# Kernel tuning notes

Measured on AMD Instinct MI355X. Metric: run time of the kernel, lower is better.

Reference implementation:

```python
import jax, jax.numpy as jnp
import numpy as np

ALPHA = 0.2          # LeakyReLU negative slope
THRESHOLD = 0.5      # adjacency threshold
NEG_INF = -9e15      # same fill value as torch source


def setup_inputs() -> dict:
    key = jax.random.key(0)
    k_in, k_adj, k_W, k_a = jax.random.split(key, 4)
    B, N, C = 32, 1024, 64
    inp = jax.random.normal(k_in, (B, N, C), dtype=jnp.float32)
    adj = jax.random.uniform(k_adj, (N, N), dtype=jnp.float32)
    # xavier_uniform with gain=1.414 (as in torch init)
    gain = 1.414
    lim_W = gain * np.sqrt(6.0 / (C + C))
    W = jax.random.uniform(k_W, (C, C), dtype=jnp.float32, minval=-lim_W, maxval=lim_W)
    lim_a = gain * np.sqrt(6.0 / (2 * C + 1))
    a = jax.random.uniform(k_a, (2 * C, 1), dtype=jnp.float32, minval=-lim_a, maxval=lim_a)
    return {"input": inp, "adj": adj, "W": W, "a": a}


def reference(input, adj, W, a):
    # h: [B, N, C]
    h = jnp.matmul(input, W)
    C = W.shape[0]
    a_src = a[:C, 0]   # applied to h_i (row / query node)
    a_dst = a[C:, 0]   # applied to h_j (col / neighbor node)
    # Algebraic decomposition of a^T [h_i || h_j]: outer-sum of two [B,N] vectors.
    s_src = jnp.matmul(h, a_src)  # [B, N]
    s_dst = jnp.matmul(h, a_dst)  # [B, N]
    e = jax.nn.leaky_relu(s_src[:, :, None] + s_dst[:, None, :], negative_slope=ALPHA)  # [B,N,N]
    mask = adj > THRESHOLD  # [N, N], broadcast over batch
    attention = jax.nn.softmax(jnp.where(mask[None, :, :], e, NEG_INF), axis=2)
    h_prime = jnp.matmul(attention, h)  # [B, N, C]
    return jax.nn.elu(h_prime)
```

## Files before the change

kernel.cpp:

```cpp
#include <hip/hip_runtime.h>
#include <math.h>

#define ALPHA 0.2f

constexpr int B = 32, N = 1024, C = 64;
constexpr int TI = 16;
constexpr int TJ = 64;

typedef __attribute__((ext_vector_type(8))) short short8;
typedef __attribute__((ext_vector_type(4))) float floatx4;

static __device__ __forceinline__ unsigned f32bf(float f) {
    unsigned u = __float_as_uint(f);
    return (u + 0x7FFFu + ((u >> 16) & 1u)) >> 16;
}

__global__ __launch_bounds__(256) void gat_mask(const float* __restrict__ adj,
                                                const float* __restrict__ Wm,
                                                const float* __restrict__ a,
                                                unsigned long long* __restrict__ mask64,
                                                float* __restrict__ wa)
{
    const int lane = threadIdx.x & 63;
    const int wave = threadIdx.x >> 6;
    const int id   = blockIdx.x * 4 + wave;
    const int i    = id >> 4;
    const int jc   = id & 15;
    const float av = adj[(size_t)i * N + jc * 64 + lane];
    const unsigned long long bal = __ballot(av > 0.5f);
    if (lane == 0) mask64[i * 16 + jc] = bal;

    if (blockIdx.x == 0 && wave == 0) {
        float accs = 0.f, accd = 0.f;
#pragma unroll
        for (int c4 = 0; c4 < 16; ++c4) {
            const float4 wv = *(const float4*)&Wm[lane * 64 + c4 * 4];
            const float4 as = *(const float4*)&a[c4 * 4];
            const float4 ad = *(const float4*)&a[64 + c4 * 4];
            accs = fmaf(wv.x, as.x, fmaf(wv.y, as.y, fmaf(wv.z, as.z, fmaf(wv.w, as.w, accs))));
            accd = fmaf(wv.x, ad.x, fmaf(wv.y, ad.y, fmaf(wv.z, ad.z, fmaf(wv.w, ad.w, accd))));
        }
        wa[lane] = accs;
        wa[64 + lane] = accd;
    }
}

__global__ __launch_bounds__(256) void gat_hs(const float* __restrict__ input,
                                              const float* __restrict__ Wm,
                                              const float* __restrict__ wa,
                                              unsigned short* __restrict__ hT,
                                              float* __restrict__ ssrc,
                                              float* __restrict__ sdst)
{
    __shared__ __align__(16) float ins[64 * 68];
    __shared__ __align__(16) unsigned short hsT[64 * 72];
    __shared__ float red_s[256], red_d[256];
    __shared__ float wa_l[128];

    const int tid  = threadIdx.x;
    const int lane = tid & 63;
    const int wave = tid >> 6;
    const int row0 = blockIdx.x * 64;
    const int b    = row0 >> 10;
    const int jb   = row0 & 1023;

    float wreg[64];
#pragma unroll
    for (int k = 0; k < 64; ++k) wreg[k] = Wm[k * 64 + lane];

    const float4* gin = (const float4*)(input + (size_t)row0 * 64);
#pragma unroll
    for (int s = 0; s < 4; ++s) {
        const int id = tid + 256 * s;
        *(float4*)&ins[(id >> 4) * 68 + (id & 15) * 4] = gin[id];
    }
    if (tid < 128) wa_l[tid] = wa[tid];
    __syncthreads();

    for (int r = 0; r < 16; ++r) {
        const int row = wave * 16 + r;
        float acc = 0.f;
#pragma unroll
        for (int k4 = 0; k4 < 16; ++k4) {
            const float4 iv = *(const float4*)&ins[row * 68 + k4 * 4];
            acc = fmaf(iv.x, wreg[k4 * 4 + 0], acc);
            acc = fmaf(iv.y, wreg[k4 * 4 + 1], acc);
            acc = fmaf(iv.z, wreg[k4 * 4 + 2], acc);
            acc = fmaf(iv.w, wreg[k4 * 4 + 3], acc);
        }
        hsT[lane * 72 + row] = (unsigned short)f32bf(acc);
    }

    {
        const int r = tid & 63, kq = tid >> 6;
        float as = 0.f, ad = 0.f;
#pragma unroll
        for (int t = 0; t < 4; ++t) {
            const float4 iv = *(const float4*)&ins[r * 68 + kq * 16 + t * 4];
            const float4 ws = *(const float4*)&wa_l[kq * 16 + t * 4];
            const float4 wd = *(const float4*)&wa_l[64 + kq * 16 + t * 4];
            as = fmaf(iv.x, ws.x, fmaf(iv.y, ws.y, fmaf(iv.z, ws.z, fmaf(iv.w, ws.w, as))));
            ad = fmaf(iv.x, wd.x, fmaf(iv.y, wd.y, fmaf(iv.z, wd.z, fmaf(iv.w, wd.w, ad))));
        }
        red_s[tid] = as;
        red_d[tid] = ad;
    }
    __syncthreads();

    if (tid < 64) {
        ssrc[row0 + tid] = red_s[tid] + red_s[tid + 64] + red_s[tid + 128] + red_s[tid + 192];
        sdst[row0 + tid] = red_d[tid] + red_d[tid + 64] + red_d[tid + 128] + red_d[tid + 192];
    }

    {
        const int c = tid >> 2, part = tid & 3;
        const short8 v0 = *(const short8*)&hsT[c * 72 + part * 16];
        const short8 v1 = *(const short8*)&hsT[c * 72 + part * 16 + 8];
        const size_t g = ((size_t)(b * 64 + c)) * 1024 + jb + part * 16;
        *(short8*)&hT[g] = v0;
        *(short8*)&hT[g + 8] = v1;
    }
}

__global__ __launch_bounds__(256) void gat_attn(const unsigned short* __restrict__ hTg,
                                                const float* __restrict__ ssrc,
                                                const float* __restrict__ sdst,
                                                const unsigned* __restrict__ mask32,
                                                float* __restrict__ out)
{
    __shared__ __align__(16) unsigned short h_u[64 * 64];
    __shared__ __align__(16) unsigned short p_u[16 * 64];
    __shared__ float psum_s[16];

    const int tid  = threadIdx.x;
    const int lane = tid & 63;
    const int wave = tid >> 6;
    const int b    = blockIdx.x & 31;
    const int i0   = (blockIdx.x >> 5) * TI;

    const int ii = tid >> 4;
    const int jq = tid & 15;
    const float ssq = ssrc[b * N + i0 + ii];
    const unsigned short* hTb = hTg + (size_t)b * 64 * 1024;
    const float* sd = sdst + b * N;
    const unsigned* mrow = mask32 + (size_t)(i0 + ii) * 32;

    const int c = tid >> 2, m2 = tid & 3;
    const int hw0 = c * 64 + (((m2 * 2)    ) ^ (c & 7)) * 8;
    const int hw1 = c * 64 + (((m2 * 2 + 1)) ^ (c & 7)) * 8;
    const int pwi = ii * 64 + ((jq >> 1) ^ (ii & 7)) * 8 + (jq & 1) * 4;
    const int fa_ii = lane & 15, fq = lane >> 4;
    const int cB = wave * 16 + (lane & 15);

    floatx4 acc = {0.f, 0.f, 0.f, 0.f};
    float psacc = 0.f;

    for (int jt = 0; jt < 16; ++jt) {
        const short8 g0 = *(const short8*)&hTb[(size_t)c * 1024 + jt * 64 + m2 * 16];
        const short8 g1 = *(const short8*)&hTb[(size_t)c * 1024 + jt * 64 + m2 * 16 + 8];
        const float4 sd4 = *(const float4*)&sd[jt * 64 + jq * 4];
        const unsigned bits = mrow[jt * 2 + (jq >> 3)] >> ((jq & 7) * 4);

        __syncthreads();
        *(short8*)&h_u[hw0] = g0;
        *(short8*)&h_u[hw1] = g1;

        float e0 = ssq + sd4.x; e0 = e0 > 0.f ? e0 : ALPHA * e0;
        float e1 = ssq + sd4.y; e1 = e1 > 0.f ? e1 : ALPHA * e1;
        float e2 = ssq + sd4.z; e2 = e2 > 0.f ? e2 : ALPHA * e2;
        float e3 = ssq + sd4.w; e3 = e3 > 0.f ? e3 : ALPHA * e3;
        const float p0 = (bits & 1u) ? __expf(e0) : 0.f;
        const float p1 = (bits & 2u) ? __expf(e1) : 0.f;
        const float p2 = (bits & 4u) ? __expf(e2) : 0.f;
        const float p3 = (bits & 8u) ? __expf(e3) : 0.f;
        psacc += (p0 + p1) + (p2 + p3);
        const uint2 pw = {f32bf(p0) | (f32bf(p1) << 16), f32bf(p2) | (f32bf(p3) << 16)};
        *(uint2*)&p_u[pwi] = pw;
        __syncthreads();

#pragma unroll
        for (int t = 0; t < 2; ++t) {
            const short8 af = *(const short8*)&p_u[fa_ii * 64 + ((t * 4 + fq) ^ (fa_ii & 7)) * 8];
            const short8 bf = *(const short8*)&h_u[cB * 64 + ((t * 4 + fq) ^ (cB & 7)) * 8];
            acc = __builtin_amdgcn_mfma_f32_16x16x32_bf16(af, bf, acc, 0, 0, 0);
        }
    }

#pragma unroll
    for (int off = 1; off < 16; off <<= 1) psacc += __shfl_xor(psacc, off, 64);
    if ((tid & 15) == 0) psum_s[ii] = psacc;
    __syncthreads();

#pragma unroll
    for (int r = 0; r < 4; ++r) {
        const int row = fq * 4 + r;
        const float hp = acc[r] / psum_s[row];
        const float o = hp > 0.f ? hp : __expf(hp) - 1.f;
        out[((size_t)(b * N + i0 + row)) * 64 + wave * 16 + (lane & 15)] = o;
    }
}

extern "C" void kernel_launch(void* const* d_in, const int* in_sizes, int n_in,
                              void* d_out, int out_size, void* d_ws, size_t ws_size,
                              hipStream_t stream) {
    const float* input = (const float*)d_in[0];
    const float* adj   = (const float*)d_in[1];
    const float* Wm    = (const float*)d_in[2];
    const float* a     = (const float*)d_in[3];
    float* out = (float*)d_out;

    char* ws = (char*)d_ws;
    unsigned short* hT = (unsigned short*)ws;
    float* ssrc = (float*)(ws + 4194304);
    float* sdst = (float*)(ws + 4194304 + 131072);
    unsigned long long* mask64 = (unsigned long long*)(ws + 4194304 + 2 * 131072);
    float* wa = (float*)(ws + 4194304 + 3 * 131072);

    gat_mask<<<N * N / 64 / 4, 256, 0, stream>>>(adj, Wm, a, mask64, wa);
    gat_hs<<<B * N / 64, 256, 0, stream>>>(input, Wm, wa, hT, ssrc, sdst);
    gat_attn<<<(N / TI) * B, 256, 0, stream>>>(hT, ssrc, sdst, (const unsigned*)mask64, out);
}
```

Before: 96.98 us.

## Split attention j-range across waves with register-direct MFMA operands and LDS reduction

The attention kernel is restructured so that each of the four waves handles a disjoint quarter of the neighbor tiles for all 64 output channels. Probabilities are built directly in MFMA A-operand registers and H tiles are loaded straight from global memory into B-operand registers, which removes the per-tile LDS staging and the two barriers per iteration. Partial accumulators and row sums are combined through shared memory once at the end. Scores are prescaled by log2(e) in the projection kernel so the hardware exp2 can be used, bf16 packing uses v_cvt_pk_bf16_f32, and the block-to-(batch,row) mapping is changed. The trade-offs are higher register pressure and uncoalesced strided global loads of H.

```diff
diff --git a/kernel.cpp b/kernel.cpp
--- a/kernel.cpp
+++ b/kernel.cpp
@@ -2,10 +2,10 @@
 #include <math.h>
 
 #define ALPHA 0.2f
+#define LOG2E 1.4426950408889634f
 
 constexpr int B = 32, N = 1024, C = 64;
 constexpr int TI = 16;
-constexpr int TJ = 64;
 
 typedef __attribute__((ext_vector_type(8))) short short8;
 typedef __attribute__((ext_vector_type(4))) float floatx4;
@@ -108,8 +108,8 @@
     __syncthreads();
 
     if (tid < 64) {
-        ssrc[row0 + tid] = red_s[tid] + red_s[tid + 64] + red_s[tid + 128] + red_s[tid + 192];
-        sdst[row0 + tid] = red_d[tid] + red_d[tid + 64] + red_d[tid + 128] + red_d[tid + 192];
+        ssrc[row0 + tid] = (red_s[tid] + red_s[tid + 64] + red_s[tid + 128] + red_s[tid + 192]) * LOG2E;
+        sdst[row0 + tid] = (red_d[tid] + red_d[tid + 64] + red_d[tid + 128] + red_d[tid + 192]) * LOG2E;
     }
 
     {
@@ -128,76 +128,131 @@
                                                 const unsigned* __restrict__ mask32,
                                                 float* __restrict__ out)
 {
-    __shared__ __align__(16) unsigned short h_u[64 * 64];
-    __shared__ __align__(16) unsigned short p_u[16 * 64];
-    __shared__ float psum_s[16];
+    __shared__ __align__(16) float red[4][16][64];
+    __shared__ float pps[4][16];
 
     const int tid  = threadIdx.x;
     const int lane = tid & 63;
-    const int wave = tid >> 6;
-    const int b    = blockIdx.x & 31;
-    const int i0   = (blockIdx.x >> 5) * TI;
-
-    const int ii = tid >> 4;
-    const int jq = tid & 15;
-    const float ssq = ssrc[b * N + i0 + ii];
+    const int w    = tid >> 6;
+    const int b    = blockIdx.x >> 6;
+    const int i0   = (blockIdx.x & 63) * TI;
+
+    const int il = lane & 15;
+    const int fq = lane >> 4;
+
+    const float ssq = ssrc[b * N + i0 + il];
+    const float* sd = sdst + b * N;
     const unsigned short* hTb = hTg + (size_t)b * 64 * 1024;
-    const float* sd = sdst + b * N;
-    const unsigned* mrow = mask32 + (size_t)(i0 + ii) * 32;
-
-    const int c = tid >> 2, m2 = tid & 3;
-    const int hw0 = c * 64 + (((m2 * 2)    ) ^ (c & 7)) * 8;
-    const int hw1 = c * 64 + (((m2 * 2 + 1)) ^ (c & 7)) * 8;
-    const int pwi = ii * 64 + ((jq >> 1) ^ (ii & 7)) * 8 + (jq & 1) * 4;
-    const int fa_ii = lane & 15, fq = lane >> 4;
-    const int cB = wave * 16 + (lane & 15);
-
-    floatx4 acc = {0.f, 0.f, 0.f, 0.f};
-    float psacc = 0.f;
-
-    for (int jt = 0; jt < 16; ++jt) {
-        const short8 g0 = *(const short8*)&hTb[(size_t)c * 1024 + jt * 64 + m2 * 16];
-        const short8 g1 = *(const short8*)&hTb[(size_t)c * 1024 + jt * 64 + m2 * 16 + 8];
-        const float4 sd4 = *(const float4*)&sd[jt * 64 + jq * 4];
-        const unsigned bits = mrow[jt * 2 + (jq >> 3)] >> ((jq & 7) * 4);
-
-        __syncthreads();
-        *(short8*)&h_u[hw0] = g0;
-        *(short8*)&h_u[hw1] = g1;
-
-        float e0 = ssq + sd4.x; e0 = e0 > 0.f ? e0 : ALPHA * e0;
-        float e1 = ssq + sd4.y; e1 = e1 > 0.f ? e1 : ALPHA * e1;
-        float e2 = ssq + sd4.z; e2 = e2 > 0.f ? e2 : ALPHA * e2;
-        float e3 = ssq + sd4.w; e3 = e3 > 0.f ? e3 : ALPHA * e3;
-        const float p0 = (bits & 1u) ? __expf(e0) : 0.f;
-        const float p1 = (bits & 2u) ? __expf(e1) : 0.f;
-        const float p2 = (bits & 4u) ? __expf(e2) : 0.f;
-        const float p3 = (bits & 8u) ? __expf(e3) : 0.f;
-        psacc += (p0 + p1) + (p2 + p3);
-        const uint2 pw = {f32bf(p0) | (f32bf(p1) << 16), f32bf(p2) | (f32bf(p3) << 16)};
-        *(uint2*)&p_u[pwi] = pw;
-        __syncthreads();
-
+    const unsigned* mrow = mask32 + (size_t)(i0 + il) * 32;
+    const int fsh = fq * 8;
+
+    floatx4 acc0 = {0.f, 0.f, 0.f, 0.f};
+    floatx4 acc1 = acc0, acc2 = acc0, acc3 = acc0;
+    float ps = 0.f;
+
+    float4 sv[2][4];
+    unsigned mv[2][2];
+    auto LDP = [&](int buf, int it) {
+        const int jt = it * 4 + w;
+        const int k0 = jt * 64 + fsh;
+        sv[buf][0] = *(const float4*)&sd[k0];
+        sv[buf][1] = *(const float4*)&sd[k0 + 4];
+        sv[buf][2] = *(const float4*)&sd[k0 + 32];
+        sv[buf][3] = *(const float4*)&sd[k0 + 36];
+        mv[buf][0] = mrow[jt * 2]     >> fsh;
+        mv[buf][1] = mrow[jt * 2 + 1] >> fsh;
+    };
+    LDP(0, 0);
+
+#pragma unroll
+    for (int it = 0; it < 4; ++it) {
+        const int cur = it & 1;
+        const int jt = it * 4 + w;
+        const unsigned short* hp = hTb + jt * 64 + fsh;
+
+        const short8 bf0 = *(const short8*)&hp[(size_t)il * 1024];
+        const short8 bf1 = *(const short8*)&hp[(size_t)il * 1024 + 32];
+        const short8 bf2 = *(const short8*)&hp[(size_t)(16 + il) * 1024];
+        const short8 bf3 = *(const short8*)&hp[(size_t)(16 + il) * 1024 + 32];
+        const short8 bf4 = *(const short8*)&hp[(size_t)(32 + il) * 1024];
+        const short8 bf5 = *(const short8*)&hp[(size_t)(32 + il) * 1024 + 32];
+        const short8 bf6 = *(const short8*)&hp[(size_t)(48 + il) * 1024];
+        const short8 bf7 = *(const short8*)&hp[(size_t)(48 + il) * 1024 + 32];
+
+        if (it < 3) LDP(cur ^ 1, it + 1);
+
+        float sdv[16];
+        *(float4*)&sdv[0]  = sv[cur][0];
+        *(float4*)&sdv[4]  = sv[cur][1];
+        *(float4*)&sdv[8]  = sv[cur][2];
+        *(float4*)&sdv[12] = sv[cur][3];
+
+        float p[16];
 #pragma unroll
         for (int t = 0; t < 2; ++t) {
-            const short8 af = *(const short8*)&p_u[fa_ii * 64 + ((t * 4 + fq) ^ (fa_ii & 7)) * 8];
-            const short8 bf = *(const short8*)&h_u[cB * 64 + ((t * 4 + fq) ^ (cB & 7)) * 8];
-            acc = __builtin_amdgcn_mfma_f32_16x16x32_bf16(af, bf, acc, 0, 0, 0);
-        }
-    }
-
-#pragma unroll
-    for (int off = 1; off < 16; off <<= 1) psacc += __shfl_xor(psacc, off, 64);
-    if ((tid & 15) == 0) psum_s[ii] = psacc;
+            const unsigned mb = mv[cur][t];
+#pragma unroll
+            for (int e = 0; e < 8; ++e) {
+                float x = ssq + sdv[t * 8 + e];
+                x = fmaxf(x, ALPHA * x);
+                x = __builtin_amdgcn_exp2f(x);
+                p[t * 8 + e] = ((mb >> e) & 1u) ? x : 0.f;
+            }
+        }
+
+        ps += ((p[0] + p[1]) + (p[2] + p[3])) + ((p[4] + p[5]) + (p[6] + p[7]))
+            + ((p[8] + p[9]) + (p[10] + p[11])) + ((p[12] + p[13]) + (p[14] + p[15]));
+
+        union { short8 v; unsigned u[4]; } af0, af1;
+#pragma unroll
+        for (int q = 0; q < 4; ++q) {
+            unsigned r0, r1;
+            asm("v_cvt_pk_bf16_f32 %0, %1, %2" : "=v"(r0) : "v"(p[q * 2]),     "v"(p[q * 2 + 1]));
+            asm("v_cvt_pk_bf16_f32 %0, %1, %2" : "=v"(r1) : "v"(p[8 + q * 2]), "v"(p[8 + q * 2 + 1]));
+            af0.u[q] = r0;
+            af1.u[q] = r1;
+        }
+
+        acc0 = __builtin_amdgcn_mfma_f32_16x16x32_bf16(af0.v, bf0, acc0, 0, 0, 0);
+        acc0 = __builtin_amdgcn_mfma_f32_16x16x32_bf16(af1.v, bf1, acc0, 0, 0, 0);
+        acc1 = __builtin_amdgcn_mfma_f32_16x16x32_bf16(af0.v, bf2, acc1, 0, 0, 0);
+        acc1 = __builtin_amdgcn_mfma_f32_16x16x32_bf16(af1.v, bf3, acc1, 0, 0, 0);
+        acc2 = __builtin_amdgcn_mfma_f32_16x16x32_bf16(af0.v, bf4, acc2, 0, 0, 0);
+        acc2 = __builtin_amdgcn_mfma_f32_16x16x32_bf16(af1.v, bf5, acc2, 0, 0, 0);
+        acc3 = __builtin_amdgcn_mfma_f32_16x16x32_bf16(af0.v, bf6, acc3, 0, 0, 0);
+        acc3 = __builtin_amdgcn_mfma_f32_16x16x32_bf16(af1.v, bf7, acc3, 0, 0, 0);
+    }
+
+    ps += __shfl_xor(ps, 16);
+    ps += __shfl_xor(ps, 32);
+    if (lane < 16) pps[w][lane] = ps;
+
+#pragma unroll
+    for (int r = 0; r < 4; ++r) {
+        red[w][fq * 4 + r][il]      = acc0[r];
+        red[w][fq * 4 + r][16 + il] = acc1[r];
+        red[w][fq * 4 + r][32 + il] = acc2[r];
+        red[w][fq * 4 + r][48 + il] = acc3[r];
+    }
     __syncthreads();
 
-#pragma unroll
-    for (int r = 0; r < 4; ++r) {
-        const int row = fq * 4 + r;
-        const float hp = acc[r] / psum_s[row];
-        const float o = hp > 0.f ? hp : __expf(hp) - 1.f;
-        out[((size_t)(b * N + i0 + row)) * 64 + wave * 16 + (lane & 15)] = o;
-    }
+    const int row = tid >> 4;
+    const int c4  = (tid & 15) * 4;
+    const float4 v0 = *(const float4*)&red[0][row][c4];
+    const float4 v1 = *(const float4*)&red[1][row][c4];
+    const float4 v2 = *(const float4*)&red[2][row][c4];
+    const float4 v3 = *(const float4*)&red[3][row][c4];
+    const float inv = 1.f / (pps[0][row] + pps[1][row] + pps[2][row] + pps[3][row]);
+    float4 o;
+    o.x = ((v0.x + v1.x) + (v2.x + v3.x)) * inv;
+    o.y = ((v0.y + v1.y) + (v2.y + v3.y)) * inv;
+    o.z = ((v0.z + v1.z) + (v2.z + v3.z)) * inv;
+    o.w = ((v0.w + v1.w) + (v2.w + v3.w)) * inv;
+    o.x = o.x > 0.f ? o.x : __expf(o.x) - 1.f;
+    o.y = o.y > 0.f ? o.y : __expf(o.y) - 1.f;
+    o.z = o.z > 0.f ? o.z : __expf(o.z) - 1.f;
+    o.w = o.w > 0.f ? o.w : __expf(o.w) - 1.f;
+    *(float4*)&out[((size_t)(b * N + i0 + row)) * 64 + c4] = o;
 }
 
 extern "C" void kernel_launch(void* const* d_in, const int* in_sizes, int n_in,
```

After: 114.8 us. +18.3%, slower.

## Pre-swizzle h into MFMA fragment layout and split j across waves

Applied to the files above, without the earlier changes.

gat_hs now writes h in a layout that matches the MFMA B-fragment order, so gat_attn loads its operands straight into registers and no longer stages tiles through LDS or calls __syncthreads per tile. Each block handles 32 query rows, and the four waves each take a disjoint quarter of the j tiles, then reduce partial accumulators and row sums through LDS at the end. The scores are prescaled by log2(e) so the kernel can use exp2 directly, and bf16 packing uses the hardware cvt_pk instruction. In exchange it needs more registers and a final cross-wave LDS reduction.

```diff
diff --git a/kernel.cpp b/kernel.cpp
--- a/kernel.cpp
+++ b/kernel.cpp
@@ -2,10 +2,10 @@
 #include <math.h>
 
 #define ALPHA 0.2f
+#define LOG2E 1.4426950408889634f
 
 constexpr int B = 32, N = 1024, C = 64;
-constexpr int TI = 16;
-constexpr int TJ = 64;
+constexpr int TI = 32;
 
 typedef __attribute__((ext_vector_type(8))) short short8;
 typedef __attribute__((ext_vector_type(4))) float floatx4;
@@ -48,7 +48,7 @@
 __global__ __launch_bounds__(256) void gat_hs(const float* __restrict__ input,
                                               const float* __restrict__ Wm,
                                               const float* __restrict__ wa,
-                                              unsigned short* __restrict__ hT,
+                                              unsigned short* __restrict__ hT2,
                                               float* __restrict__ ssrc,
                                               float* __restrict__ sdst)
 {
@@ -108,96 +108,151 @@
     __syncthreads();
 
     if (tid < 64) {
-        ssrc[row0 + tid] = red_s[tid] + red_s[tid + 64] + red_s[tid + 128] + red_s[tid + 192];
-        sdst[row0 + tid] = red_d[tid] + red_d[tid + 64] + red_d[tid + 128] + red_d[tid + 192];
+        ssrc[row0 + tid] = (red_s[tid] + red_s[tid + 64] + red_s[tid + 128] + red_s[tid + 192]) * LOG2E;
+        sdst[row0 + tid] = (red_d[tid] + red_d[tid + 64] + red_d[tid + 128] + red_d[tid + 192]) * LOG2E;
     }
 
     {
-        const int c = tid >> 2, part = tid & 3;
-        const short8 v0 = *(const short8*)&hsT[c * 72 + part * 16];
-        const short8 v1 = *(const short8*)&hsT[c * 72 + part * 16 + 8];
-        const size_t g = ((size_t)(b * 64 + c)) * 1024 + jb + part * 16;
-        *(short8*)&hT[g] = v0;
-        *(short8*)&hT[g + 8] = v1;
-    }
-}
-
-__global__ __launch_bounds__(256) void gat_attn(const unsigned short* __restrict__ hTg,
+        const int il2 = (tid & 7) * 2;
+        const int fq  = (tid >> 3) & 3;
+        const int cg  = (tid >> 5) & 3;
+        const int t   = tid >> 7;
+        const int c   = cg * 16 + il2;
+        const int off = t * 32 + fq * 8;
+        const short8 v0 = *(const short8*)&hsT[c * 72 + off];
+        const short8 v1 = *(const short8*)&hsT[(c + 1) * 72 + off];
+        unsigned short* g = hT2 + (((size_t)b * 16 + (jb >> 6)) << 12) + tid * 16;
+        *(short8*)&g[0] = v0;
+        *(short8*)&g[8] = v1;
+    }
+}
+
+__global__ __launch_bounds__(256) void gat_attn(const unsigned short* __restrict__ hT2,
                                                 const float* __restrict__ ssrc,
                                                 const float* __restrict__ sdst,
                                                 const unsigned* __restrict__ mask32,
                                                 float* __restrict__ out)
 {
-    __shared__ __align__(16) unsigned short h_u[64 * 64];
-    __shared__ __align__(16) unsigned short p_u[16 * 64];
-    __shared__ float psum_s[16];
+    __shared__ __align__(16) float red[4][TI][68];
+    __shared__ float pps[4][2][16];
 
     const int tid  = threadIdx.x;
     const int lane = tid & 63;
-    const int wave = tid >> 6;
-    const int b    = blockIdx.x & 31;
-    const int i0   = (blockIdx.x >> 5) * TI;
-
-    const int ii = tid >> 4;
-    const int jq = tid & 15;
-    const float ssq = ssrc[b * N + i0 + ii];
-    const unsigned short* hTb = hTg + (size_t)b * 64 * 1024;
+    const int w    = tid >> 6;
+    const int b    = blockIdx.x >> 5;
+    const int i0   = (blockIdx.x & 31) * TI;
+
+    const int il = lane & 15;
+    const int fq = lane >> 4;
+
+    const float ssq0 = ssrc[b * N + i0 + il];
+    const float ssq1 = ssrc[b * N + i0 + 16 + il];
     const float* sd = sdst + b * N;
-    const unsigned* mrow = mask32 + (size_t)(i0 + ii) * 32;
-
-    const int c = tid >> 2, m2 = tid & 3;
-    const int hw0 = c * 64 + (((m2 * 2)    ) ^ (c & 7)) * 8;
-    const int hw1 = c * 64 + (((m2 * 2 + 1)) ^ (c & 7)) * 8;
-    const int pwi = ii * 64 + ((jq >> 1) ^ (ii & 7)) * 8 + (jq & 1) * 4;
-    const int fa_ii = lane & 15, fq = lane >> 4;
-    const int cB = wave * 16 + (lane & 15);
-
-    floatx4 acc = {0.f, 0.f, 0.f, 0.f};
-    float psacc = 0.f;
-
-    for (int jt = 0; jt < 16; ++jt) {
-        const short8 g0 = *(const short8*)&hTb[(size_t)c * 1024 + jt * 64 + m2 * 16];
-        const short8 g1 = *(const short8*)&hTb[(size_t)c * 1024 + jt * 64 + m2 * 16 + 8];
-        const float4 sd4 = *(const float4*)&sd[jt * 64 + jq * 4];
-        const unsigned bits = mrow[jt * 2 + (jq >> 3)] >> ((jq & 7) * 4);
-
-        __syncthreads();
-        *(short8*)&h_u[hw0] = g0;
-        *(short8*)&h_u[hw1] = g1;
-
-        float e0 = ssq + sd4.x; e0 = e0 > 0.f ? e0 : ALPHA * e0;
-        float e1 = ssq + sd4.y; e1 = e1 > 0.f ? e1 : ALPHA * e1;
-        float e2 = ssq + sd4.z; e2 = e2 > 0.f ? e2 : ALPHA * e2;
-        float e3 = ssq + sd4.w; e3 = e3 > 0.f ? e3 : ALPHA * e3;
-        const float p0 = (bits & 1u) ? __expf(e0) : 0.f;
-        const float p1 = (bits & 2u) ? __expf(e1) : 0.f;
-        const float p2 = (bits & 4u) ? __expf(e2) : 0.f;
-        const float p3 = (bits & 8u) ? __expf(e3) : 0.f;
-        psacc += (p0 + p1) + (p2 + p3);
-        const uint2 pw = {f32bf(p0) | (f32bf(p1) << 16), f32bf(p2) | (f32bf(p3) << 16)};
-        *(uint2*)&p_u[pwi] = pw;
-        __syncthreads();
-
-#pragma unroll
-        for (int t = 0; t < 2; ++t) {
-            const short8 af = *(const short8*)&p_u[fa_ii * 64 + ((t * 4 + fq) ^ (fa_ii & 7)) * 8];
-            const short8 bf = *(const short8*)&h_u[cB * 64 + ((t * 4 + fq) ^ (cB & 7)) * 8];
-            acc = __builtin_amdgcn_mfma_f32_16x16x32_bf16(af, bf, acc, 0, 0, 0);
-        }
-    }
-
-#pragma unroll
-    for (int off = 1; off < 16; off <<= 1) psacc += __shfl_xor(psacc, off, 64);
-    if ((tid & 15) == 0) psum_s[ii] = psacc;
+    const unsigned* mb0 = mask32 + (size_t)(i0 + il) * 32;
+    const unsigned* mb1 = mask32 + (size_t)(i0 + 16 + il) * 32;
+
+    floatx4 acc[2][4];
+#pragma unroll
+    for (int ig = 0; ig < 2; ++ig)
+#pragma unroll
+        for (int cg = 0; cg < 4; ++cg) acc[ig][cg] = (floatx4){0.f, 0.f, 0.f, 0.f};
+    float ps0 = 0.f, ps1 = 0.f;
+
+    union Af { short8 v; unsigned u[4]; };
+
+    for (int it = 0; it < 4; ++it) {
+        const int jt = it * 4 + w;
+        const float4 s0 = *(const float4*)&sd[jt * 64 + fq * 8];
+        const float4 s1 = *(const float4*)&sd[jt * 64 + fq * 8 + 4];
+        const float4 s2 = *(const float4*)&sd[jt * 64 + 32 + fq * 8];
+        const float4 s3 = *(const float4*)&sd[jt * 64 + 32 + fq * 8 + 4];
+        const uint2 m0 = *(const uint2*)&mb0[jt * 2];
+        const uint2 m1 = *(const uint2*)&mb1[jt * 2];
+        const unsigned short* hp = hT2 + (((size_t)b * 16 + jt) << 12) + lane * 8;
+        short8 bf[4][2];
+#pragma unroll
+        for (int cg = 0; cg < 4; ++cg) {
+            bf[cg][0] = *(const short8*)(hp + (0 * 4 + cg) * 512);
+            bf[cg][1] = *(const short8*)(hp + (1 * 4 + cg) * 512);
+        }
+
+        float sv[16];
+        *(float4*)&sv[0]  = s0;
+        *(float4*)&sv[4]  = s1;
+        *(float4*)&sv[8]  = s2;
+        *(float4*)&sv[12] = s3;
+
+        Af af[2][2];
+#pragma unroll
+        for (int ig = 0; ig < 2; ++ig) {
+            const float ssq = ig ? ssq1 : ssq0;
+            const uint2 mw = ig ? m1 : m0;
+            float psl = 0.f;
+#pragma unroll
+            for (int t = 0; t < 2; ++t) {
+                const unsigned mbits = (t ? mw.y : mw.x) >> (fq * 8);
+                float p[8];
+#pragma unroll
+                for (int e = 0; e < 8; ++e) {
+                    float x = ssq + sv[t * 8 + e];
+                    x = fmaxf(x, ALPHA * x);
+                    x = __builtin_amdgcn_exp2f(x);
+                    p[e] = ((mbits >> e) & 1u) ? x : 0.f;
+                }
+                psl += ((p[0] + p[1]) + (p[2] + p[3])) + ((p[4] + p[5]) + (p[6] + p[7]));
+#pragma unroll
+                for (int q = 0; q < 4; ++q) {
+                    unsigned r;
+                    asm("v_cvt_pk_bf16_f32 %0, %1, %2" : "=v"(r) : "v"(p[q * 2]), "v"(p[q * 2 + 1]));
+                    af[ig][t].u[q] = r;
+                }
+            }
+            if (ig) ps1 += psl; else ps0 += psl;
+        }
+
+#pragma unroll
+        for (int ig = 0; ig < 2; ++ig)
+#pragma unroll
+            for (int cg = 0; cg < 4; ++cg) {
+                acc[ig][cg] = __builtin_amdgcn_mfma_f32_16x16x32_bf16(af[ig][0].v, bf[cg][0], acc[ig][cg], 0, 0, 0);
+                acc[ig][cg] = __builtin_amdgcn_mfma_f32_16x16x32_bf16(af[ig][1].v, bf[cg][1], acc[ig][cg], 0, 0, 0);
+            }
+    }
+
+    ps0 += __shfl_xor(ps0, 16); ps0 += __shfl_xor(ps0, 32);
+    ps1 += __shfl_xor(ps1, 16); ps1 += __shfl_xor(ps1, 32);
+    if (lane < 16) { pps[w][0][lane] = ps0; pps[w][1][lane] = ps1; }
+
+#pragma unroll
+    for (int ig = 0; ig < 2; ++ig)
+#pragma unroll
+        for (int cg = 0; cg < 4; ++cg)
+#pragma unroll
+            for (int r = 0; r < 4; ++r)
+                red[w][ig * 16 + fq * 4 + r][cg * 16 + il] = acc[ig][cg][r];
     __syncthreads();
 
-#pragma unroll
-    for (int r = 0; r < 4; ++r) {
-        const int row = fq * 4 + r;
-        const float hp = acc[r] / psum_s[row];
-        const float o = hp > 0.f ? hp : __expf(hp) - 1.f;
-        out[((size_t)(b * N + i0 + row)) * 64 + wave * 16 + (lane & 15)] = o;
-    }
+    const int row = tid >> 3;
+    const int c0  = (tid & 7) * 8;
+    float4 oa = {0.f, 0.f, 0.f, 0.f}, ob = {0.f, 0.f, 0.f, 0.f};
+#pragma unroll
+    for (int ww = 0; ww < 4; ++ww) {
+        const float4 xa = *(const float4*)&red[ww][row][c0];
+        const float4 xb = *(const float4*)&red[ww][row][c0 + 4];
+        oa.x += xa.x; oa.y += xa.y; oa.z += xa.z; oa.w += xa.w;
+        ob.x += xb.x; ob.y += xb.y; ob.z += xb.z; ob.w += xb.w;
+    }
+    const int ig = row >> 4, rl = row & 15;
+    const float inv = 1.f / (pps[0][ig][rl] + pps[1][ig][rl] + pps[2][ig][rl] + pps[3][ig][rl]);
+    float o[8] = {oa.x, oa.y, oa.z, oa.w, ob.x, ob.y, ob.z, ob.w};
+#pragma unroll
+    for (int e = 0; e < 8; ++e) {
+        const float hp = o[e] * inv;
+        o[e] = hp > 0.f ? hp : __expf(hp) - 1.f;
+    }
+    float* op = out + ((size_t)(b * N + i0 + row)) * 64 + c0;
+    *(float4*)&op[0] = *(float4*)&o[0];
+    *(float4*)&op[4] = *(float4*)&o[4];
 }
 
 extern "C" void kernel_launch(void* const* d_in, const int* in_sizes, int n_in,
@@ -210,13 +265,13 @@
     float* out = (float*)d_out;
 
     char* ws = (char*)d_ws;
-    unsigned short* hT = (unsigned short*)ws;
+    unsigned short* hT2 = (unsigned short*)ws;
     float* ssrc = (float*)(ws + 4194304);
     float* sdst = (float*)(ws + 4194304 + 131072);
     unsigned long long* mask64 = (unsigned long long*)(ws + 4194304 + 2 * 131072);
     float* wa = (float*)(ws + 4194304 + 3 * 131072);
 
     gat_mask<<<N * N / 64 / 4, 256, 0, stream>>>(adj, Wm, a, mask64, wa);
-    gat_hs<<<B * N / 64, 256, 0, stream>>>(input, Wm, wa, hT, ssrc, sdst);
-    gat_attn<<<(N / TI) * B, 256, 0, stream>>>(hT, ssrc, sdst, (const unsigned*)mask64, out);
-}
+    gat_hs<<<B * N / 64, 256, 0, stream>>>(input, Wm, wa, hT2, ssrc, sdst);
+    gat_attn<<<B * (N / TI), 256, 0, stream>>>(hT2, ssrc, sdst, (const unsigned*)mask64, out);
+}
```

New measurement: 90.38 us. 1.07x faster.
